# Performance work log

Hardware: AMD Instinct MI355X
Metric: run time of the kernel (lower is better)

Reference implementation:

```python
import jax, jax.numpy as jnp
import numpy as np

N, E = 50000, 800000
IN_CH, OUT_CH = 128, 16
H1, D1 = 2, 2 * OUT_CH           # conv1: heads=2, per-head dim 32, concat -> 64
MID = H1 * D1                    # 64
NEG_SLOPE = 0.2

def setup_inputs() -> dict:
    key = jax.random.key(0)
    ks = jax.random.split(key, 16)
    s = lambda k, shape: jax.random.normal(k, shape, dtype=jnp.float32) * 0.1
    return {
        "x": jax.random.normal(ks[0], (N, IN_CH), dtype=jnp.float32),
        "edge_index": jax.random.randint(ks[1], (2, E), 0, N, dtype=jnp.int64),
        "W1": s(ks[2], (IN_CH, H1 * D1)),
        "att_src1": s(ks[3], (H1, D1)),
        "att_dst1": s(ks[4], (H1, D1)),
        "b1": jnp.zeros((MID,), jnp.float32),
        "W_mu": s(ks[5], (MID, OUT_CH)),
        "att_src_mu": s(ks[6], (1, OUT_CH)),
        "att_dst_mu": s(ks[7], (1, OUT_CH)),
        "b_mu": jnp.zeros((OUT_CH,), jnp.float32),
        "W_ls": s(ks[8], (MID, OUT_CH)),
        "att_src_ls": s(ks[9], (1, OUT_CH)),
        "att_dst_ls": s(ks[10], (1, OUT_CH)),
        "b_ls": jnp.zeros((OUT_CH,), jnp.float32),
    }

def gat_conv(x, src, dst, W, att_src, att_dst, bias, heads, d):
    # x: [N, F]; src/dst: [E'] (self loops included); PyG GATConv, eval mode (dropout off)
    n = x.shape[0]
    h = (x @ W).reshape(n, heads, d)                     # [N, H, D]
    a_src = jnp.sum(h * att_src, axis=-1)                # [N, H]
    a_dst = jnp.sum(h * att_dst, axis=-1)                # [N, H]
    e = jax.nn.leaky_relu(a_src[src] + a_dst[dst], NEG_SLOPE)   # [E', H]
    # segment softmax over incoming edges of each destination node
    m = jax.ops.segment_max(e, dst, num_segments=n)
    ex = jnp.exp(e - m[dst])
    denom = jax.ops.segment_sum(ex, dst, num_segments=n)
    alpha = ex / (denom[dst] + 1e-16)                    # [E', H]
    msg = h[src] * alpha[:, :, None]                     # [E', H, D]
    out = jax.ops.segment_sum(msg, dst, num_segments=n)  # [N, H, D]
    return out, bias

def reference(x, edge_index, W1, att_src1, att_dst1, b1,
              W_mu, att_src_mu, att_dst_mu, b_mu,
              W_ls, att_src_ls, att_dst_ls, b_ls):
    n = x.shape[0]
    loops = jnp.arange(n, dtype=edge_index.dtype)
    src = jnp.concatenate([edge_index[0], loops])        # add_self_loops=True (inputs have none)
    dst = jnp.concatenate([edge_index[1], loops])
    h, b = gat_conv(x, src, dst, W1, att_src1, att_dst1, b1, H1, D1)
    h = jax.nn.relu(h.reshape(n, H1 * D1) + b)           # concat=True -> [N, 64]
    mu, bm = gat_conv(h, src, dst, W_mu, att_src_mu, att_dst_mu, b_mu, 1, OUT_CH)
    ls, bl = gat_conv(h, src, dst, W_ls, att_src_ls, att_dst_ls, b_ls, 1, OUT_CH)
    mu = mu.mean(axis=1) + bm                            # concat=False, heads=1 -> mean == squeeze
    ls = ls.mean(axis=1) + bl
    return (mu, ls)
```

## Files before the change

### kernel.cpp

```cpp
#include <hip/hip_runtime.h>

#define NEG 0.2f

__device__ __forceinline__ float lrelu(float v) { return v > 0.f ? v : NEG * v; }

__device__ __forceinline__ unsigned short f2bf(float f) {
    unsigned u = __float_as_uint(f);
    unsigned r = (u + 0x7FFF + ((u >> 16) & 1)) >> 16;
    return (unsigned short)r;
}
__device__ __forceinline__ float bf_lo(unsigned v) { return __uint_as_float(v << 16); }
__device__ __forceinline__ float bf_hi(unsigned v) { return __uint_as_float(v & 0xffff0000u); }

__global__ void build_w1ext(const float* __restrict__ W1, const float* __restrict__ asrc,
                            const float* __restrict__ adst, float* __restrict__ Wext) {
    int i = blockIdx.x * blockDim.x + threadIdx.x;
    if (i >= 128 * 68) return;
    int k = i / 68, c = i % 68;
    if (c < 64) { Wext[i] = W1[k * 64 + c]; return; }
    int j = c - 64;
    int hh = j & 1;
    const float* att = (j >= 2) ? adst : asrc;
    float s = 0.f;
    for (int d = 0; d < 32; ++d) s += W1[k * 64 + hh * 32 + d] * att[hh * 32 + d];
    Wext[i] = s;
}

__global__ void build_w2ext(const float* __restrict__ Wmu, const float* __restrict__ Wls,
                            const float* __restrict__ asmu, const float* __restrict__ admu,
                            const float* __restrict__ asls, const float* __restrict__ adls,
                            float* __restrict__ Wext) {
    int i = blockIdx.x * blockDim.x + threadIdx.x;
    if (i >= 64 * 36) return;
    int k = i / 36, c = i % 36;
    if (c < 16) { Wext[i] = Wmu[k * 16 + c]; return; }
    if (c < 32) { Wext[i] = Wls[k * 16 + (c - 16)]; return; }
    int j = c - 32;
    const float* W = (j < 2) ? Wmu : Wls;
    const float* att = (j == 0) ? asmu : (j == 1) ? admu : (j == 2) ? asls : adls;
    float s = 0.f;
    for (int c2 = 0; c2 < 16; ++c2) s += W[k * 16 + c2] * att[c2];
    Wext[i] = s;
}

__global__ __launch_bounds__(256) void gemm1(const float* __restrict__ x,
                                             const float* __restrict__ Wext,
                                             unsigned* __restrict__ h32, float* __restrict__ a1, int n) {
    __shared__ float xs[16][129];
    __shared__ float Ws[128][68];
    int t = threadIdx.x;
    int row0 = blockIdx.x * 16;
    for (int i = t; i < 128 * 68; i += 256) Ws[i / 68][i % 68] = Wext[i];
    for (int i = t; i < 16 * 128; i += 256) {
        int r = i >> 7, k = i & 127;
        int gr = row0 + r;
        xs[r][k] = (gr < n) ? x[gr * 128 + k] : 0.f;
    }
    __syncthreads();
    int r = t >> 4, c = t & 15;
    float acc0 = 0, acc1 = 0, acc2 = 0, acc3 = 0;
    for (int k = 0; k < 128; ++k) {
        float xv = xs[r][k];
        acc0 += xv * Ws[k][c * 4 + 0];
        acc1 += xv * Ws[k][c * 4 + 1];
        acc2 += xv * Ws[k][c * 4 + 2];
        acc3 += xv * Ws[k][c * 4 + 3];
    }
    int gr = row0 + r;
    if (gr < n) {
        unsigned p0 = ((unsigned)f2bf(acc1) << 16) | f2bf(acc0);
        unsigned p1 = ((unsigned)f2bf(acc3) << 16) | f2bf(acc2);
        *(uint2*)&h32[gr * 32 + c * 2] = make_uint2(p0, p1);
    }
    if (t < 64) {
        int r2 = t >> 2, j = t & 3;
        float a = 0.f;
        for (int k = 0; k < 128; ++k) a += xs[r2][k] * Ws[k][64 + j];
        if (row0 + r2 < n) a1[(row0 + r2) * 4 + j] = a;
    }
}

__global__ void count_deg(const int* __restrict__ dstv, int E, int* __restrict__ deg) {
    int i = blockIdx.x * blockDim.x + threadIdx.x;
    if (i < E) atomicAdd(&deg[dstv[i]], 1);
}

__global__ __launch_bounds__(256) void block_sums(const int* __restrict__ deg, int n,
                                                  int* __restrict__ bsums) {
    int i = blockIdx.x * 256 + threadIdx.x;
    int v = (i < n) ? deg[i] : 0;
    for (int o = 32; o > 0; o >>= 1) v += __shfl_down(v, o, 64);
    __shared__ int ws[4];
    if ((threadIdx.x & 63) == 0) ws[threadIdx.x >> 6] = v;
    __syncthreads();
    if (threadIdx.x == 0) bsums[blockIdx.x] = ws[0] + ws[1] + ws[2] + ws[3];
}

__global__ __launch_bounds__(256) void scan_bsums(int* __restrict__ bsums, int nb) {
    __shared__ int s[256];
    int t = threadIdx.x;
    int v = (t < nb) ? bsums[t] : 0;
    s[t] = v;
    __syncthreads();
    for (int o = 1; o < 256; o <<= 1) {
        int u = (t >= o) ? s[t - o] : 0;
        __syncthreads();
        s[t] += u;
        __syncthreads();
    }
    if (t < nb) bsums[t] = s[t] - v;
}

__global__ __launch_bounds__(256) void write_offs(const int* __restrict__ deg,
                                                  const int* __restrict__ bsums, int n,
                                                  int* __restrict__ offs, int* __restrict__ cursor) {
    int t = threadIdx.x;
    int i = blockIdx.x * 256 + t;
    int v = (i < n) ? deg[i] : 0;
    __shared__ int s[256];
    s[t] = v;
    __syncthreads();
    for (int o = 1; o < 256; o <<= 1) {
        int u = (t >= o) ? s[t - o] : 0;
        __syncthreads();
        s[t] += u;
        __syncthreads();
    }
    int excl = s[t] - v + bsums[blockIdx.x];
    if (i < n) { offs[i] = excl; cursor[i] = excl; }
    if (i == n - 1) offs[n] = excl + v;
}

__global__ void scatter_edges(const int* __restrict__ srcv, const int* __restrict__ dstv, int E,
                              int* __restrict__ cursor, int* __restrict__ srcs) {
    int i = blockIdx.x * blockDim.x + threadIdx.x;
    if (i < E) {
        int d = dstv[i];
        int slot = atomicAdd(&cursor[d], 1);
        srcs[slot] = srcv[i];
    }
}

__global__ __launch_bounds__(256) void agg1(const unsigned* __restrict__ h32, const float* __restrict__ a1,
                                            const int* __restrict__ offs, const int* __restrict__ srcs,
                                            const float* __restrict__ b1, float* __restrict__ h1, int n) {
    int wid = threadIdx.x >> 6, lane = threadIdx.x & 63;
    int node = blockIdx.x * 4 + wid;
    if (node >= n) return;
    int half = lane >> 5;
    int l = lane & 31;
    int head = l >> 4;
    float adst = a1[node * 4 + 2 + head];
    float acc0 = 0.f, acc1 = 0.f, denom = 0.f;
    if (half == 0) {
        float w = __expf(lrelu(a1[node * 4 + head] + adst));
        unsigned hv = h32[node * 32 + l];
        acc0 = w * bf_lo(hv); acc1 = w * bf_hi(hv);
        denom = w;
    }
    int kb = offs[node], ke = offs[node + 1];
    for (int k = kb + half; k < ke; k += 2) {
        int s = srcs[k];
        float wv = __expf(lrelu(a1[s * 4 + head] + adst));
        unsigned hv = h32[s * 32 + l];
        denom += wv;
        acc0 += wv * bf_lo(hv);
        acc1 += wv * bf_hi(hv);
    }
    acc0  += __shfl(acc0,  lane ^ 32, 64);
    acc1  += __shfl(acc1,  lane ^ 32, 64);
    denom += __shfl(denom, lane ^ 32, 64);
    if (half == 0) {
        float o0 = acc0 / denom + b1[2 * l];
        float o1 = acc1 / denom + b1[2 * l + 1];
        *(float2*)&h1[node * 64 + 2 * l] = make_float2(fmaxf(o0, 0.f), fmaxf(o1, 0.f));
    }
}

__global__ __launch_bounds__(256) void gemm2(const float* __restrict__ h1,
                                             const float* __restrict__ Wext,
                                             unsigned* __restrict__ hml, float* __restrict__ a2, int n) {
    __shared__ float hs[16][65];
    __shared__ float Ws[64][36];
    int t = threadIdx.x;
    int row0 = blockIdx.x * 16;
    for (int i = t; i < 64 * 36; i += 256) Ws[i / 36][i % 36] = Wext[i];
    for (int i = t; i < 16 * 64; i += 256) {
        int r = i >> 6, k = i & 63;
        int gr = row0 + r;
        hs[r][k] = (gr < n) ? h1[gr * 64 + k] : 0.f;
    }
    __syncthreads();
    int r = t >> 4, c = t & 15;
    float am = 0, al = 0;
    for (int k = 0; k < 64; ++k) {
        float hv = hs[r][k];
        am += hv * Ws[k][c];
        al += hv * Ws[k][16 + c];
    }
    int gr = row0 + r;
    if (gr < n) hml[gr * 16 + c] = ((unsigned)f2bf(al) << 16) | f2bf(am);
    if (t < 64) {
        int r2 = t >> 2, j = t & 3;
        float a = 0.f;
        for (int k = 0; k < 64; ++k) a += hs[r2][k] * Ws[k][32 + j];
        if (row0 + r2 < n) a2[(row0 + r2) * 4 + j] = a;
    }
}

__global__ __launch_bounds__(256) void agg2(const unsigned* __restrict__ hml,
                                            const float* __restrict__ a2, const int* __restrict__ offs,
                                            const int* __restrict__ srcs,
                                            const float* __restrict__ bmu, const float* __restrict__ bls,
                                            float* __restrict__ out, int n) {
    int grp = threadIdx.x >> 5;
    int node = blockIdx.x * 8 + grp;
    if (node >= n) return;
    int lane32 = threadIdx.x & 31;
    int half = lane32 >> 4;
    int c = lane32 & 15;
    float admu = a2[node * 4 + 1], adls = a2[node * 4 + 3];
    float amu = 0.f, als = 0.f, dmu = 0.f, dls = 0.f;
    if (half == 0) {
        float wmu = __expf(lrelu(a2[node * 4 + 0] + admu));
        float wls = __expf(lrelu(a2[node * 4 + 2] + adls));
        unsigned hv = hml[node * 16 + c];
        amu = wmu * bf_lo(hv); als = wls * bf_hi(hv);
        dmu = wmu; dls = wls;
    }
    int kb = offs[node], ke = offs[node + 1];
    for (int k = kb + half; k < ke; k += 2) {
        int s = srcs[k];
        float4 av = *(const float4*)&a2[s * 4];
        float w1v = __expf(lrelu(av.x + admu));
        float w2v = __expf(lrelu(av.z + adls));
        unsigned hv = hml[s * 16 + c];
        dmu += w1v; dls += w2v;
        amu += w1v * bf_lo(hv);
        als += w2v * bf_hi(hv);
    }
    amu += __shfl_xor(amu, 16, 64);
    als += __shfl_xor(als, 16, 64);
    dmu += __shfl_xor(dmu, 16, 64);
    dls += __shfl_xor(dls, 16, 64);
    if (half == 0) {
        out[node * 16 + c] = amu / dmu + bmu[c];
        out[(size_t)n * 16 + node * 16 + c] = als / dls + bls[c];
    }
}

extern "C" void kernel_launch(void* const* d_in, const int* in_sizes, int n_in,
                              void* d_out, int out_size, void* d_ws, size_t ws_size,
                              hipStream_t stream) {
    const float* x    = (const float*)d_in[0];
    const int*   ei   = (const int*)d_in[1];
    const float* W1   = (const float*)d_in[2];
    const float* as1  = (const float*)d_in[3];
    const float* ad1  = (const float*)d_in[4];
    const float* b1   = (const float*)d_in[5];
    const float* Wmu  = (const float*)d_in[6];
    const float* asmu = (const float*)d_in[7];
    const float* admu = (const float*)d_in[8];
    const float* bmu  = (const float*)d_in[9];
    const float* Wls  = (const float*)d_in[10];
    const float* asls = (const float*)d_in[11];
    const float* adls = (const float*)d_in[12];
    const float* bls  = (const float*)d_in[13];
    float* out = (float*)d_out;

    int n = in_sizes[0] / 128;
    int E = in_sizes[1] / 2;

    char* ws = (char*)d_ws;
    size_t off = 0;
    auto alloc = [&](size_t b) { size_t p = off; off = (off + b + 255) & ~(size_t)255; return p; };

    unsigned* h32 = (unsigned*)(ws + alloc((size_t)n * 32 * 4));
    float*    h1  = (float*)(ws + alloc((size_t)n * 64 * 4));
    float*    a1  = (float*)(ws + alloc((size_t)n * 4 * 4));
    unsigned* hml = (unsigned*)(ws + alloc((size_t)n * 16 * 4));
    float*    a2  = (float*)(ws + alloc((size_t)n * 4 * 4));
    float*    w1e = (float*)(ws + alloc(128 * 68 * 4));
    float*    w2e = (float*)(ws + alloc(64 * 36 * 4));
    int*   deg    = (int*)(ws + alloc((size_t)n * 4));
    int*   offs   = (int*)(ws + alloc((size_t)(n + 1) * 4));
    int*   cursor = (int*)(ws + alloc((size_t)n * 4));
    int*   srcs   = (int*)(ws + alloc((size_t)E * 4));
    int*   bsums  = (int*)(ws + alloc(1024 * 4));

    int nb = (n + 255) / 256;

    hipMemsetAsync(deg, 0, (size_t)n * 4, stream);
    build_w1ext<<<(128 * 68 + 255) / 256, 256, 0, stream>>>(W1, as1, ad1, w1e);
    build_w2ext<<<(64 * 36 + 255) / 256, 256, 0, stream>>>(Wmu, Wls, asmu, admu, asls, adls, w2e);
    gemm1<<<(n + 15) / 16, 256, 0, stream>>>(x, w1e, h32, a1, n);
    count_deg<<<(E + 255) / 256, 256, 0, stream>>>(ei + E, E, deg);
    block_sums<<<nb, 256, 0, stream>>>(deg, n, bsums);
    scan_bsums<<<1, 256, 0, stream>>>(bsums, nb);
    write_offs<<<nb, 256, 0, stream>>>(deg, bsums, n, offs, cursor);
    scatter_edges<<<(E + 255) / 256, 256, 0, stream>>>(ei, ei + E, E, cursor, srcs);
    agg1<<<(n + 3) / 4, 256, 0, stream>>>(h32, a1, offs, srcs, b1, h1, n);
    gemm2<<<(n + 15) / 16, 256, 0, stream>>>(h1, w2e, hml, a2, n);
    agg2<<<(n + 7) / 8, 256, 0, stream>>>(hml, a2, offs, srcs, bmu, bls, out, n);
}
```

Measured before the change: 334.5 us.

## Retile gemm1 with 4x4 register tiles and build CSR via two-level bucket sort

gemm1 now processes 64 rows per block with 320 threads, each computing a 4x4 output tile from float4 shared-memory loads. The attention projection columns are padded into the same tile to remove the separate serial loop. CSR construction replaces per-node degree counting, a multi-kernel scan and per-node atomic scatter with coarse 16-node buckets, one single-block scan, and a per-bucket local sort in shared memory. This reduces global atomic contention and launch count, at the cost of an extra E×8-byte pairs buffer pass.

```diff
diff --git a/kernel.cpp b/kernel.cpp
--- a/kernel.cpp
+++ b/kernel.cpp
@@ -15,9 +15,10 @@
 __global__ void build_w1ext(const float* __restrict__ W1, const float* __restrict__ asrc,
                             const float* __restrict__ adst, float* __restrict__ Wext) {
     int i = blockIdx.x * blockDim.x + threadIdx.x;
-    if (i >= 128 * 68) return;
-    int k = i / 68, c = i % 68;
+    if (i >= 128 * 80) return;
+    int k = i / 80, c = i % 80;
     if (c < 64) { Wext[i] = W1[k * 64 + c]; return; }
+    if (c >= 68) { Wext[i] = 0.f; return; }
     int j = c - 64;
     int hh = j & 1;
     const float* att = (j >= 2) ? adst : asrc;
@@ -43,101 +44,128 @@
     Wext[i] = s;
 }
 
-__global__ __launch_bounds__(256) void gemm1(const float* __restrict__ x,
+__global__ __launch_bounds__(320) void gemm1(const float* __restrict__ x,
                                              const float* __restrict__ Wext,
                                              unsigned* __restrict__ h32, float* __restrict__ a1, int n) {
-    __shared__ float xs[16][129];
-    __shared__ float Ws[128][68];
+    __shared__ float xs[64][132];
+    __shared__ float Ws[128][80];
     int t = threadIdx.x;
-    int row0 = blockIdx.x * 16;
-    for (int i = t; i < 128 * 68; i += 256) Ws[i / 68][i % 68] = Wext[i];
-    for (int i = t; i < 16 * 128; i += 256) {
-        int r = i >> 7, k = i & 127;
+    int row0 = blockIdx.x * 64;
+    for (int i = t; i < 128 * 20; i += 320) {
+        int r = i / 20, cq = i % 20;
+        *(float4*)&Ws[r][cq * 4] = *(const float4*)&Wext[r * 80 + cq * 4];
+    }
+    for (int i = t; i < 64 * 32; i += 320) {
+        int r = i >> 5, kq = i & 31;
         int gr = row0 + r;
-        xs[r][k] = (gr < n) ? x[gr * 128 + k] : 0.f;
-    }
-    __syncthreads();
-    int r = t >> 4, c = t & 15;
-    float acc0 = 0, acc1 = 0, acc2 = 0, acc3 = 0;
-    for (int k = 0; k < 128; ++k) {
-        float xv = xs[r][k];
-        acc0 += xv * Ws[k][c * 4 + 0];
-        acc1 += xv * Ws[k][c * 4 + 1];
-        acc2 += xv * Ws[k][c * 4 + 2];
-        acc3 += xv * Ws[k][c * 4 + 3];
-    }
-    int gr = row0 + r;
-    if (gr < n) {
-        unsigned p0 = ((unsigned)f2bf(acc1) << 16) | f2bf(acc0);
-        unsigned p1 = ((unsigned)f2bf(acc3) << 16) | f2bf(acc2);
-        *(uint2*)&h32[gr * 32 + c * 2] = make_uint2(p0, p1);
-    }
-    if (t < 64) {
-        int r2 = t >> 2, j = t & 3;
-        float a = 0.f;
-        for (int k = 0; k < 128; ++k) a += xs[r2][k] * Ws[k][64 + j];
-        if (row0 + r2 < n) a1[(row0 + r2) * 4 + j] = a;
-    }
-}
-
-__global__ void count_deg(const int* __restrict__ dstv, int E, int* __restrict__ deg) {
+        float4 v = (gr < n) ? *(const float4*)&x[gr * 128 + kq * 4] : make_float4(0, 0, 0, 0);
+        *(float4*)&xs[r][kq * 4] = v;
+    }
+    __syncthreads();
+    int rg = t / 20, cg = t % 20;
+    int r0 = rg * 4, c0 = cg * 4;
+    float4 acc0 = make_float4(0, 0, 0, 0), acc1 = acc0, acc2 = acc0, acc3 = acc0;
+    for (int k = 0; k < 128; k += 4) {
+        float4 w0 = *(float4*)&Ws[k + 0][c0];
+        float4 w1 = *(float4*)&Ws[k + 1][c0];
+        float4 w2 = *(float4*)&Ws[k + 2][c0];
+        float4 w3 = *(float4*)&Ws[k + 3][c0];
+#pragma unroll
+        for (int j = 0; j < 4; ++j) {
+            float4 xv = *(float4*)&xs[r0 + j][k];
+            float4& a = j == 0 ? acc0 : j == 1 ? acc1 : j == 2 ? acc2 : acc3;
+            a.x += xv.x * w0.x + xv.y * w1.x + xv.z * w2.x + xv.w * w3.x;
+            a.y += xv.x * w0.y + xv.y * w1.y + xv.z * w2.y + xv.w * w3.y;
+            a.z += xv.x * w0.z + xv.y * w1.z + xv.z * w2.z + xv.w * w3.z;
+            a.w += xv.x * w0.w + xv.y * w1.w + xv.z * w2.w + xv.w * w3.w;
+        }
+    }
+#pragma unroll
+    for (int j = 0; j < 4; ++j) {
+        int gr = row0 + r0 + j;
+        if (gr >= n) break;
+        float4 a = j == 0 ? acc0 : j == 1 ? acc1 : j == 2 ? acc2 : acc3;
+        if (cg < 16) {
+            unsigned p0 = ((unsigned)f2bf(a.y) << 16) | f2bf(a.x);
+            unsigned p1 = ((unsigned)f2bf(a.w) << 16) | f2bf(a.z);
+            *(uint2*)&h32[gr * 32 + (c0 >> 1)] = make_uint2(p0, p1);
+        } else if (cg == 16) {
+            *(float4*)&a1[gr * 4] = a;
+        }
+    }
+}
+
+__global__ void bucket_count(const int* __restrict__ dstv, int E, int* __restrict__ bcnt) {
     int i = blockIdx.x * blockDim.x + threadIdx.x;
-    if (i < E) atomicAdd(&deg[dstv[i]], 1);
-}
-
-__global__ __launch_bounds__(256) void block_sums(const int* __restrict__ deg, int n,
-                                                  int* __restrict__ bsums) {
-    int i = blockIdx.x * 256 + threadIdx.x;
-    int v = (i < n) ? deg[i] : 0;
-    for (int o = 32; o > 0; o >>= 1) v += __shfl_down(v, o, 64);
-    __shared__ int ws[4];
-    if ((threadIdx.x & 63) == 0) ws[threadIdx.x >> 6] = v;
-    __syncthreads();
-    if (threadIdx.x == 0) bsums[blockIdx.x] = ws[0] + ws[1] + ws[2] + ws[3];
-}
-
-__global__ __launch_bounds__(256) void scan_bsums(int* __restrict__ bsums, int nb) {
-    __shared__ int s[256];
+    if (i < E) atomicAdd(&bcnt[dstv[i] >> 4], 1);
+}
+
+__global__ __launch_bounds__(1024) void scan_buckets(const int* __restrict__ bcnt, int nbuck,
+                                                     int* __restrict__ bstart, int* __restrict__ bcur,
+                                                     int* __restrict__ offs, int n, int E) {
+    __shared__ int s[1024];
     int t = threadIdx.x;
-    int v = (t < nb) ? bsums[t] : 0;
-    s[t] = v;
-    __syncthreads();
-    for (int o = 1; o < 256; o <<= 1) {
+    int v0[4];
+    int lsum = 0;
+#pragma unroll
+    for (int j = 0; j < 4; ++j) {
+        int i = t * 4 + j;
+        v0[j] = (i < nbuck) ? bcnt[i] : 0;
+        lsum += v0[j];
+    }
+    s[t] = lsum;
+    __syncthreads();
+    for (int o = 1; o < 1024; o <<= 1) {
         int u = (t >= o) ? s[t - o] : 0;
         __syncthreads();
         s[t] += u;
         __syncthreads();
     }
-    if (t < nb) bsums[t] = s[t] - v;
-}
-
-__global__ __launch_bounds__(256) void write_offs(const int* __restrict__ deg,
-                                                  const int* __restrict__ bsums, int n,
-                                                  int* __restrict__ offs, int* __restrict__ cursor) {
-    int t = threadIdx.x;
-    int i = blockIdx.x * 256 + t;
-    int v = (i < n) ? deg[i] : 0;
-    __shared__ int s[256];
-    s[t] = v;
-    __syncthreads();
-    for (int o = 1; o < 256; o <<= 1) {
-        int u = (t >= o) ? s[t - o] : 0;
-        __syncthreads();
-        s[t] += u;
-        __syncthreads();
-    }
-    int excl = s[t] - v + bsums[blockIdx.x];
-    if (i < n) { offs[i] = excl; cursor[i] = excl; }
-    if (i == n - 1) offs[n] = excl + v;
-}
-
-__global__ void scatter_edges(const int* __restrict__ srcv, const int* __restrict__ dstv, int E,
-                              int* __restrict__ cursor, int* __restrict__ srcs) {
+    int base = s[t] - lsum;
+#pragma unroll
+    for (int j = 0; j < 4; ++j) {
+        int i = t * 4 + j;
+        if (i < nbuck) { bstart[i] = base; bcur[i] = base; }
+        base += v0[j];
+    }
+    if (t == 1023) { bstart[nbuck] = E; offs[n] = E; }
+}
+
+__global__ void bucket_scatter(const int* __restrict__ srcv, const int* __restrict__ dstv, int E,
+                               int* __restrict__ bcur, int2* __restrict__ pairs) {
     int i = blockIdx.x * blockDim.x + threadIdx.x;
     if (i < E) {
         int d = dstv[i];
-        int slot = atomicAdd(&cursor[d], 1);
-        srcs[slot] = srcv[i];
+        int slot = atomicAdd(&bcur[d >> 4], 1);
+        pairs[slot] = make_int2(srcv[i], d);
+    }
+}
+
+__global__ __launch_bounds__(256) void build_csr(const int2* __restrict__ pairs,
+                                                 const int* __restrict__ bstart, int n,
+                                                 int* __restrict__ offs, int* __restrict__ srcs) {
+    int b = blockIdx.x;
+    int base = bstart[b], cnt = bstart[b + 1] - base;
+    __shared__ int hist[16], curs[16];
+    int t = threadIdx.x;
+    if (t < 16) hist[t] = 0;
+    __syncthreads();
+    for (int i = t; i < cnt; i += 256) atomicAdd(&hist[pairs[base + i].y & 15], 1);
+    __syncthreads();
+    if (t == 0) {
+        int s = 0;
+#pragma unroll
+        for (int j = 0; j < 16; ++j) { int h = hist[j]; hist[j] = s; curs[j] = s; s += h; }
+    }
+    __syncthreads();
+    if (t < 16) {
+        int node = b * 16 + t;
+        if (node < n) offs[node] = base + hist[t];
+    }
+    for (int i = t; i < cnt; i += 256) {
+        int2 p = pairs[base + i];
+        int slot = atomicAdd(&curs[p.y & 15], 1);
+        srcs[base + slot] = p.x;
     }
 }
 
@@ -270,6 +298,7 @@
 
     int n = in_sizes[0] / 128;
     int E = in_sizes[1] / 2;
+    int nbuck = (n + 15) >> 4;
 
     char* ws = (char*)d_ws;
     size_t off = 0;
@@ -280,25 +309,23 @@
     float*    a1  = (float*)(ws + alloc((size_t)n * 4 * 4));
     unsigned* hml = (unsigned*)(ws + alloc((size_t)n * 16 * 4));
     float*    a2  = (float*)(ws + alloc((size_t)n * 4 * 4));
-    float*    w1e = (float*)(ws + alloc(128 * 68 * 4));
+    float*    w1e = (float*)(ws + alloc(128 * 80 * 4));
     float*    w2e = (float*)(ws + alloc(64 * 36 * 4));
-    int*   deg    = (int*)(ws + alloc((size_t)n * 4));
     int*   offs   = (int*)(ws + alloc((size_t)(n + 1) * 4));
-    int*   cursor = (int*)(ws + alloc((size_t)n * 4));
     int*   srcs   = (int*)(ws + alloc((size_t)E * 4));
-    int*   bsums  = (int*)(ws + alloc(1024 * 4));
-
-    int nb = (n + 255) / 256;
-
-    hipMemsetAsync(deg, 0, (size_t)n * 4, stream);
-    build_w1ext<<<(128 * 68 + 255) / 256, 256, 0, stream>>>(W1, as1, ad1, w1e);
+    int*   bcnt   = (int*)(ws + alloc((size_t)nbuck * 4));
+    int*   bstart = (int*)(ws + alloc((size_t)(nbuck + 1) * 4));
+    int*   bcur   = (int*)(ws + alloc((size_t)nbuck * 4));
+    int2*  pairs  = (int2*)(ws + alloc((size_t)E * 8));
+
+    hipMemsetAsync(bcnt, 0, (size_t)nbuck * 4, stream);
+    build_w1ext<<<(128 * 80 + 255) / 256, 256, 0, stream>>>(W1, as1, ad1, w1e);
     build_w2ext<<<(64 * 36 + 255) / 256, 256, 0, stream>>>(Wmu, Wls, asmu, admu, asls, adls, w2e);
-    gemm1<<<(n + 15) / 16, 256, 0, stream>>>(x, w1e, h32, a1, n);
-    count_deg<<<(E + 255) / 256, 256, 0, stream>>>(ei + E, E, deg);
-    block_sums<<<nb, 256, 0, stream>>>(deg, n, bsums);
-    scan_bsums<<<1, 256, 0, stream>>>(bsums, nb);
-    write_offs<<<nb, 256, 0, stream>>>(deg, bsums, n, offs, cursor);
-    scatter_edges<<<(E + 255) / 256, 256, 0, stream>>>(ei, ei + E, E, cursor, srcs);
+    gemm1<<<(n + 63) / 64, 320, 0, stream>>>(x, w1e, h32, a1, n);
+    bucket_count<<<(E + 255) / 256, 256, 0, stream>>>(ei + E, E, bcnt);
+    scan_buckets<<<1, 1024, 0, stream>>>(bcnt, nbuck, bstart, bcur, offs, n, E);
+    bucket_scatter<<<(E + 255) / 256, 256, 0, stream>>>(ei, ei + E, E, bcur, pairs);
+    build_csr<<<nbuck, 256, 0, stream>>>(pairs, bstart, n, offs, srcs);
     agg1<<<(n + 3) / 4, 256, 0, stream>>>(h32, a1, offs, srcs, b1, h1, n);
     gemm2<<<(n + 15) / 16, 256, 0, stream>>>(h1, w2e, hml, a2, n);
     agg2<<<(n + 7) / 8, 256, 0, stream>>>(hml, a2, offs, srcs, bmu, bls, out, n);
```

Result: slower. 388.4 us (+16.1%).
